# Optimization experiments

Hardware: AMD Instinct MI355X
Metric: run time of the kernel (lower is better)

Reference implementation:

```python
import jax, jax.numpy as jnp
import numpy as np

D_M = 1024
NUM_TOK = 4096


def setup_inputs() -> dict:
    key = jax.random.key(0)
    ks = jax.random.split(key, 7)
    mk = lambda k, shp: jax.random.normal(k, shp, dtype=jnp.float32) * 0.02
    return {
        "X": jax.random.normal(ks[0], (D_M, NUM_TOK), dtype=jnp.float32),
        "W_Q": mk(ks[1], (D_M, D_M)),
        "W_K": mk(ks[2], (D_M, D_M)),
        "W_V": mk(ks[3], (D_M, D_M)),
        "W_O": mk(ks[4], (D_M, D_M)),
        "mlp_in": mk(ks[5], (D_M, D_M)),
        "mlp_out": mk(ks[6], (D_M, D_M)),
    }


def reference(X, W_Q, W_K, W_V, W_O, mlp_in, mlp_out):
    # X: [d_m, num_tok]; module transposes to tokens-major [N, d]
    Xt = X.T  # [N, d]
    N = Xt.shape[0]
    Q = Xt @ W_Q  # [N, d]
    K = Xt @ W_K  # [N, d]
    scores = Q @ K.T  # [N, N] -- NOTE: no 1/sqrt(d) scaling, as in the original
    causal = jnp.tril(jnp.ones((N, N), dtype=bool))  # keep lower triangle incl. diag
    scores = jnp.where(causal, scores, -jnp.inf)
    A = jax.nn.softmax(scores, axis=-1)  # [N, N]
    # original applies W_V then W_O to X BEFORE the attention mix
    RH = (Xt @ W_V) @ W_O  # [N, d]
    Xt = Xt + A @ RH  # residual + attention
    h = jax.nn.relu(Xt @ mlp_in)  # [N, d] (hidden dim == d_m in original)
    Xt = Xt + h @ mlp_out  # residual + MLP
    return Xt.T  # back to [d_m, num_tok]
```

## Files before the change

### kernel.cpp

```cpp
#include <hip/hip_runtime.h>
#include <stdint.h>
#include <stddef.h>

using f16 = _Float16;
typedef __attribute__((ext_vector_type(8))) _Float16 f16x8;
typedef __attribute__((ext_vector_type(4))) float f32x4;

__device__ __forceinline__ void async_copy16(const f16* g, f16* l) {
    __builtin_amdgcn_global_load_lds(
        (const __attribute__((address_space(1))) void*)g,
        (__attribute__((address_space(3))) void*)l, 16, 0, 0);
}

template <int N>
__device__ __forceinline__ void wait_vmcnt() {
    if constexpr (N == 0)       asm volatile("s_waitcnt vmcnt(0)" ::: "memory");
    else if constexpr (N == 6)  asm volatile("s_waitcnt vmcnt(6)" ::: "memory");
    else if constexpr (N == 8)  asm volatile("s_waitcnt vmcnt(8)" ::: "memory");
}

__device__ __forceinline__ void hard_barrier() {
    __builtin_amdgcn_sched_barrier(0);
    __builtin_amdgcn_s_barrier();
    __builtin_amdgcn_sched_barrier(0);
}

__global__ __launch_bounds__(256)
void prep_w(const float* __restrict__ w0, const float* __restrict__ w1,
            const float* __restrict__ w2, const float* __restrict__ w3,
            const float* __restrict__ w4, const float* __restrict__ w5,
            f16* o0, f16* o1, f16* o2, f16* o3, f16* o4, f16* o5, int D) {
    __shared__ float tile[32][33];
    const int tx = threadIdx.x & 31, ty = threadIdx.x >> 5;
    const int b = blockIdx.x;
    const int z = b >> 10, r = b & 1023;
    const float* in = z == 0 ? w0 : z == 1 ? w1 : z == 2 ? w2 : z == 3 ? w3 : z == 4 ? w4 : w5;
    f16* out = z == 0 ? o0 : z == 1 ? o1 : z == 2 ? o2 : z == 3 ? o3 : z == 4 ? o4 : o5;
    const int c0 = (r & 31) * 32, r0 = (r >> 5) * 32;
    if (z < 3) {
#pragma unroll
        for (int j = 0; j < 4; j++) {
            size_t idx = (size_t)(r0 + ty + j * 8) * D + c0 + tx;
            out[idx] = (f16)in[idx];
        }
    } else {
#pragma unroll
        for (int j = 0; j < 4; j++)
            tile[ty + j * 8][tx] = in[(size_t)(r0 + ty + j * 8) * D + c0 + tx];
        __syncthreads();
#pragma unroll
        for (int j = 0; j < 4; j++)
            out[(size_t)(c0 + ty + j * 8) * D + r0 + tx] = (f16)tile[tx][ty + j * 8];
    }
}

__device__ __forceinline__ void body64db(
    f16* lds, const f16* __restrict__ A, const f16* __restrict__ B,
    f16* __restrict__ Ch, int m0, int n0, int N, int K, int lda) {
    const int t = threadIdx.x;
    const int lane = t & 63, wave = t >> 6;
    const int wm = (wave >> 1) * 32, wn = (wave & 1) * 32;
    const int lm = lane & 15, lq = lane >> 4;
    const int srow = t >> 2;
    const int gs = ((t & 3) ^ ((srow >> 1) & 3)) * 8;
    const int rs = (lq ^ ((lm >> 1) & 3)) * 8;

    auto stage = [&](f16* buf, int k0) {
#pragma unroll
        for (int r = 0; r < 4; r++)
            async_copy16(A + (size_t)(m0 + srow) * lda + k0 + r * 32 + gs,
                         buf + r * 2048 + t * 8);
#pragma unroll
        for (int r = 0; r < 4; r++)
            async_copy16(B + (size_t)(n0 + srow) * K + k0 + r * 32 + gs,
                         buf + 8192 + r * 2048 + t * 8);
    };

    f32x4 acc[2][2] = {};
    stage(lds, 0);
    __syncthreads();
    int cur = 0;
    for (int k0 = 0; k0 < K; k0 += 128) {
        f16* cb = lds + cur * 16384;
        if (k0 + 128 < K) stage(lds + (cur ^ 1) * 16384, k0 + 128);
#pragma unroll
        for (int kk = 0; kk < 4; kk++) {
            f16x8 af[2], bf[2];
#pragma unroll
            for (int i = 0; i < 2; i++)
                af[i] = *(const f16x8*)&cb[kk * 2048 + (wm + i * 16 + lm) * 32 + rs];
#pragma unroll
            for (int j = 0; j < 2; j++)
                bf[j] = *(const f16x8*)&cb[8192 + kk * 2048 + (wn + j * 16 + lm) * 32 + rs];
#pragma unroll
            for (int i = 0; i < 2; i++)
#pragma unroll
                for (int j = 0; j < 2; j++)
                    acc[i][j] = __builtin_amdgcn_mfma_f32_16x16x32_f16(
                        af[i], bf[j], acc[i][j], 0, 0, 0);
        }
        __syncthreads();
        cur ^= 1;
    }

#pragma unroll
    for (int i = 0; i < 2; i++) {
        const int row = m0 + wm + i * 16 + lq * 4;
#pragma unroll
        for (int j = 0; j < 2; j++) {
            const int col = n0 + wn + j * 16 + lm;
            f32x4 v = acc[i][j];
#pragma unroll
            for (int r = 0; r < 4; r++)
                Ch[(size_t)(row + r) * N + col] = (f16)v[r];
        }
    }
}

__global__ __launch_bounds__(256, 2)
void prepx_tiny(const float* __restrict__ X, f16* __restrict__ Xth,
                const f16* Wkh, const f16* Wqh, f16* GT,
                const f16* Wot, const f16* Wvh, f16* HT, int D, int NT) {
    __shared__ alignas(16) f16 smem[32768];
    int b = blockIdx.x;
    if (b < 4096) {
        float* tile = (float*)smem;
        const int tx = threadIdx.x & 31, ty = threadIdx.x >> 5;
        const int c0 = (b & 127) * 32, r0 = (b >> 7) * 32;
#pragma unroll
        for (int j = 0; j < 4; j++)
            tile[(ty + j * 8) * 33 + tx] = X[(size_t)(r0 + ty + j * 8) * NT + c0 + tx];
        __syncthreads();
#pragma unroll
        for (int j = 0; j < 4; j++)
            Xth[(size_t)(c0 + ty + j * 8) * D + r0 + tx] = (f16)tile[tx * 33 + ty + j * 8];
        return;
    }
    b -= 4096;
    if (b < 256)
        body64db(smem, Wkh, Wqh, GT, (b >> 4) * 64, (b & 15) * 64, 1024, 1024, 1024);
    else {
        const int r = b - 256;
        body64db(smem, Wot, Wvh, HT, (r >> 4) * 64, (r & 15) * 64, 1024, 1024, 1024);
    }
}

__global__ __launch_bounds__(256)
void softmax_rows(f16* __restrict__ A, int N) {
    const int row = blockIdx.x, len = row + 1;
    const int lim = ((row >> 7) + 1) << 7;
    f16* a = A + (size_t)row * N;
    __shared__ float red[256];
    const int t = threadIdx.x;

    float v[16];
    float mx = -1e30f;
#pragma unroll
    for (int j = 0; j < 2; j++) {
        const int c = (t + j * 256) * 8;
        if (c < len) {
            f16x8 x = *(const f16x8*)(a + c);
#pragma unroll
            for (int e = 0; e < 8; e++) {
                float f = (c + e < len) ? (float)x[e] : -1e30f;
                v[j * 8 + e] = f;
                mx = fmaxf(mx, f);
            }
        } else {
#pragma unroll
            for (int e = 0; e < 8; e++) v[j * 8 + e] = -1e30f;
        }
    }
    red[t] = mx; __syncthreads();
    for (int o = 128; o > 0; o >>= 1) { if (t < o) red[t] = fmaxf(red[t], red[t + o]); __syncthreads(); }
    mx = red[0]; __syncthreads();

    float sum = 0.f;
#pragma unroll
    for (int k = 0; k < 16; k++) {
        float e = (v[k] > -1e29f) ? __expf(v[k] - mx) : 0.0f;
        v[k] = e;
        sum += e;
    }
    red[t] = sum; __syncthreads();
    for (int o = 128; o > 0; o >>= 1) { if (t < o) red[t] += red[t + o]; __syncthreads(); }
    const float inv = 1.0f / red[0];
#pragma unroll
    for (int j = 0; j < 2; j++) {
        const int c = (t + j * 256) * 8;
        if (c < lim) {
            f16x8 o8;
#pragma unroll
            for (int e = 0; e < 8; e++) o8[e] = (f16)(v[j * 8 + e] * inv);
            *(f16x8*)(a + c) = o8;
        }
    }
}


__device__ __forceinline__ void body128sq(
    f16* lds, const f16* __restrict__ A, const f16* __restrict__ B,
    f16* __restrict__ Ch, int m0, int n0, int N, int K, int lda) {
    constexpr int BUF = 16384;
    const int t = threadIdx.x;
    const int lane = t & 63, wave = t >> 6;
    const int wm = (wave >> 1) * 64, wn = (wave & 1) * 64;
    const int lm = lane & 15, lq = lane >> 4;
    const int srow = t >> 2;
    const int gs = ((t & 3) ^ ((srow >> 1) & 3)) * 8;
    const int rs = (lq ^ ((lm >> 1) & 3)) * 8;

    f32x4 acc[4][4] = {};

    auto stage = [&](f16* buf, int k0) {
#pragma unroll
        for (int r = 0; r < 4; r++)
            async_copy16(A + (size_t)(m0 + (r & 1) * 64 + srow) * lda + k0 + (r >> 1) * 32 + gs,
                         buf + r * 2048 + t * 8);
#pragma unroll
        for (int r = 0; r < 4; r++)
            async_copy16(B + (size_t)(n0 + (r & 1) * 64 + srow) * K + k0 + (r >> 1) * 32 + gs,
                         buf + 8192 + r * 2048 + t * 8);
    };

    auto compute = [&](const f16* cb) {
#pragma unroll
        for (int kk = 0; kk < 2; kk++) {
            f16x8 af[4], bf[4];
#pragma unroll
            for (int i = 0; i < 4; i++)
                af[i] = *(const f16x8*)&cb[kk * 4096 + (wm + i * 16 + lm) * 32 + rs];
#pragma unroll
            for (int j = 0; j < 4; j++)
                bf[j] = *(const f16x8*)&cb[8192 + kk * 4096 + (wn + j * 16 + lm) * 32 + rs];
#pragma unroll
            for (int i = 0; i < 4; i++)
#pragma unroll
                for (int j = 0; j < 4; j++)
                    acc[i][j] = __builtin_amdgcn_mfma_f32_16x16x32_f16(
                        af[i], bf[j], acc[i][j], 0, 0, 0);
        }
    };

    const int NS = K >> 6;
    stage(lds, 0);
    for (int s = 0; s < NS; s++) {
        if (s + 1 < NS) {
            stage(lds + ((s + 1) & 1) * BUF, (s + 1) << 6);
            wait_vmcnt<8>();
        } else {
            wait_vmcnt<0>();
        }
        hard_barrier();
        compute(lds + (s & 1) * BUF);
        if (s + 1 < NS) hard_barrier();
    }

#pragma unroll
    for (int i = 0; i < 4; i++) {
        const int row = m0 + wm + i * 16 + lq * 4;
#pragma unroll
        for (int j = 0; j < 4; j++) {
            const int col = n0 + wn + j * 16 + lm;
            f32x4 v = acc[i][j];
#pragma unroll
            for (int r = 0; r < 4; r++)
                Ch[(size_t)(row + r) * N + col] = (f16)v[r];
        }
    }
}

template <int MODE>
__device__ __forceinline__ void body_nar2(
    f16* lds, const f16* __restrict__ A, const f16* __restrict__ B,
    float* __restrict__ Cf, f16* __restrict__ Ch, const f16* __restrict__ resid,
    int m0, int n0, int M, int N, int K, int lda, int Keff) {
    constexpr int ASZ = 128 * 64;
    constexpr int SSZ = ASZ + 64 * 64;
    const int t = threadIdx.x;
    const int lane = t & 63, wave = t >> 6;
    const int wm = (wave >> 1) * 64, wn = (wave & 1) * 32;
    const int lm = lane & 15, lq = lane >> 4;
    const int srow = t >> 2;
    const int gs = ((t & 3) ^ ((srow >> 1) & 3)) * 8;
    const int rs = (lq ^ ((lm >> 1) & 3)) * 8;

    f32x4 acc[4][2] = {};

    auto stage = [&](f16* buf, int k0) {
#pragma unroll
        for (int r = 0; r < 4; r++)
            async_copy16(A + (size_t)(m0 + (r & 1) * 64 + srow) * lda + k0 + (r >> 1) * 32 + gs,
                         buf + r * 2048 + t * 8);
#pragma unroll
        for (int r = 0; r < 2; r++)
            async_copy16(B + (size_t)(n0 + srow) * K + k0 + r * 32 + gs,
                         buf + ASZ + r * 2048 + t * 8);
    };

    auto compute = [&](const f16* cb) {
#pragma unroll
        for (int kk = 0; kk < 2; kk++) {
            f16x8 af[4], bf[2];
#pragma unroll
            for (int i = 0; i < 4; i++)
                af[i] = *(const f16x8*)&cb[kk * 4096 + (wm + i * 16 + lm) * 32 + rs];
#pragma unroll
            for (int j = 0; j < 2; j++)
                bf[j] = *(const f16x8*)&cb[ASZ + kk * 2048 + (wn + j * 16 + lm) * 32 + rs];
#pragma unroll
            for (int i = 0; i < 4; i++)
#pragma unroll
                for (int j = 0; j < 2; j++)
                    acc[i][j] = __builtin_amdgcn_mfma_f32_16x16x32_f16(
                        af[i], bf[j], acc[i][j], 0, 0, 0);
        }
    };

    stage(lds, 0);
    const int NS = Keff >> 6;
    for (int s = 0; s < NS; s++) {
        if (s + 1 < NS) {
            stage(lds + ((s + 1) & 1) * SSZ, (s + 1) << 6);
            wait_vmcnt<6>();
        } else {
            wait_vmcnt<0>();
        }
        hard_barrier();
        compute(lds + (s & 1) * SSZ);
        hard_barrier();
    }

#pragma unroll
    for (int i = 0; i < 4; i++) {
        const int row = m0 + wm + i * 16 + lq * 4;
#pragma unroll
        for (int j = 0; j < 2; j++) {
            const int col = n0 + wn + j * 16 + lm;
            f32x4 v = acc[i][j];
#pragma unroll
            for (int r = 0; r < 4; r++) {
                if (MODE == 0) {
                    Ch[(size_t)(row + r) * N + col] = (f16)v[r];
                } else if (MODE == 2) {
                    float o = v[r] + (float)resid[(size_t)(row + r) * N + col];
                    Ch[(size_t)(row + r) * N + col] = (f16)o;
                } else if (MODE == 3) {
                    Ch[(size_t)(row + r) * N + col] = (f16)fmaxf(v[r], 0.0f);
                } else {
                    float o = v[r] + (float)resid[(size_t)(row + r) * N + col];
                    Cf[(size_t)col * M + (row + r)] = o;
                }
            }
        }
    }
}

__global__ __launch_bounds__(256, 3)
void midq(const f16* Xth, const f16* GT, f16* Qp) {
    __shared__ alignas(16) f16 smem[24576];
    const int x = blockIdx.x & 7, s = blockIdx.x >> 3;
    const int m = x + 8 * (s >> 4), n = s & 15;
    body_nar2<0>(smem, Xth, GT, nullptr, Qp, nullptr,
                 m * 128, n * 64, 4096, 1024, 1024, 1024, 1024);
}

__global__ __launch_bounds__(256, 2)
void scores_midrh(const f16* Qp, const f16* Xth, f16* Af,
                  const f16* HT, f16* RHt) {
    __shared__ alignas(16) f16 smem[32768];
    int b = blockIdx.x;
    if (b < 528) {
        const int x = b & 7;
        int s = b >> 3;
        int m = 0, n = 0;
#pragma unroll
        for (int q = 3; q >= 0; q--) {
            const int mm = 8 * q + ((q & 1) ? 7 - x : x);
            if (s < mm + 1) { m = mm; n = s; break; }
            s -= mm + 1;
        }
        body128sq(smem, Qp, Xth, Af, m * 128, n * 128, 4096, 1024, 1024);
    } else {
        const int r = b - 528;
        const int x = r & 7;
        const int s = r >> 3;
        const int n = x + 8 * (s >> 3), m = s & 7;
        body128sq(smem, HT, Xth, RHt, m * 128, n * 128, 4096, 1024, 1024);
    }
}

template <int MODE, bool CAUSAL_K>
__global__ __launch_bounds__(256, 3)
void gemm_nar(const f16* __restrict__ A, const f16* __restrict__ B,
              float* __restrict__ Cf, f16* __restrict__ Ch,
              const f16* __restrict__ resid, int M, int N, int K, int lda) {
    __shared__ alignas(16) f16 smem[24576];
    const int x = blockIdx.x & 7, s = blockIdx.x >> 3;
    const int qs = s >> 4, n = s & 15;
    int m;
    if (CAUSAL_K) {
        const int q = (qs == 0) ? 3 : (qs == 1) ? 2 : (qs == 2) ? 0 : 1;
        m = 8 * q + ((q & 1) ? 7 - x : x);
    } else {
        m = x + 8 * qs;
    }
    const int m0 = m * 128, n0 = n * 64;
    int Keff = K;
    if (CAUSAL_K) {
        Keff = m0 + 128;
        if (Keff > K) Keff = K;
    }
    body_nar2<MODE>(smem, A, B, Cf, Ch, resid,
                    m0, n0, M, N, K, lda, Keff);
}

extern "C" void kernel_launch(void* const* d_in, const int* in_sizes, int n_in,
                              void* d_out, int out_size, void* d_ws, size_t ws_size,
                              hipStream_t stream) {
    const int D = 1024, NT = 4096;
    const float* X = (const float*)d_in[0];
    const float* W[6] = {(const float*)d_in[1], (const float*)d_in[2],
                         (const float*)d_in[3], (const float*)d_in[4],
                         (const float*)d_in[5], (const float*)d_in[6]};
    char* ws = (char*)d_ws;
    auto MB = [](size_t x) { return x << 20; };

    f16*   Xth  = (f16*)(ws + MB(0));
    f16*   Wqh  = (f16*)(ws + MB(8));
    f16*   Wkh  = (f16*)(ws + MB(10));
    f16*   Wvh  = (f16*)(ws + MB(12));
    f16*   Wot  = (f16*)(ws + MB(14));
    f16*   W4t  = (f16*)(ws + MB(16));
    f16*   W5t  = (f16*)(ws + MB(18));
    f16*   GT   = (f16*)(ws + MB(20));
    f16*   HT   = (f16*)(ws + MB(22));
    f16*   Qp   = (f16*)(ws + MB(24));
    f16*   Af   = (f16*)(ws + MB(32));
    f16*   RHt  = (f16*)(ws + MB(64));
    f16*   Y1h  = (f16*)(ws + MB(72));
    f16*   hb   = (f16*)(ws + MB(24));
    float* outF = (float*)d_out;

    prep_w<<<6144, 256, 0, stream>>>(W[0], W[1], W[2], W[3], W[4], W[5],
                                     Wqh, Wkh, Wvh, Wot, W4t, W5t, D);

    prepx_tiny<<<4608, 256, 0, stream>>>(X, Xth, Wkh, Wqh, GT, Wot, Wvh, HT,
                                         D, NT);

    midq<<<512, 256, 0, stream>>>(Xth, GT, Qp);

    scores_midrh<<<784, 256, 0, stream>>>(Qp, Xth, Af, HT, RHt);

    softmax_rows<<<NT, 256, 0, stream>>>(Af, NT);

    gemm_nar<2, true><<<512, 256, 0, stream>>>(
        Af, RHt, nullptr, Y1h, Xth, NT, D, NT, NT);

    gemm_nar<3, false><<<512, 256, 0, stream>>>(
        Y1h, W4t, nullptr, hb, nullptr, NT, D, D, D);

    gemm_nar<4, false><<<512, 256, 0, stream>>>(
        hb, W5t, outF, nullptr, Y1h, NT, D, D, D);
}
```

Baseline: 229.6 us.

## Use wave-per-row softmax, move MLP weight prep into scores kernel, adjust launch bounds

Softmax now assigns one 64-lane wavefront per row and reduces with shuffles instead of a 256-thread LDS tree with repeated block barriers. The exponentials are recomputed in the final pass so only raw half values need to stay in registers. The transpose/cast of the two MLP weights moves out of prep_w and into trailing blocks of the scores/RH kernel, where it can fill idle compute units. The occupancy hint for midq and gemm_nar drops from 3 to 2 blocks, which may let the compiler use more registers per thread at the cost of fewer resident blocks.

```diff
diff --git a/kernel.cpp b/kernel.cpp
--- a/kernel.cpp
+++ b/kernel.cpp
@@ -28,14 +28,13 @@
 __global__ __launch_bounds__(256)
 void prep_w(const float* __restrict__ w0, const float* __restrict__ w1,
             const float* __restrict__ w2, const float* __restrict__ w3,
-            const float* __restrict__ w4, const float* __restrict__ w5,
-            f16* o0, f16* o1, f16* o2, f16* o3, f16* o4, f16* o5, int D) {
+            f16* o0, f16* o1, f16* o2, f16* o3, int D) {
     __shared__ float tile[32][33];
     const int tx = threadIdx.x & 31, ty = threadIdx.x >> 5;
     const int b = blockIdx.x;
     const int z = b >> 10, r = b & 1023;
-    const float* in = z == 0 ? w0 : z == 1 ? w1 : z == 2 ? w2 : z == 3 ? w3 : z == 4 ? w4 : w5;
-    f16* out = z == 0 ? o0 : z == 1 ? o1 : z == 2 ? o2 : z == 3 ? o3 : z == 4 ? o4 : o5;
+    const float* in = z == 0 ? w0 : z == 1 ? w1 : z == 2 ? w2 : w3;
+    f16* out = z == 0 ? o0 : z == 1 ? o1 : z == 2 ? o2 : o3;
     const int c0 = (r & 31) * 32, r0 = (r >> 5) * 32;
     if (z < 3) {
 #pragma unroll
@@ -146,53 +145,60 @@
 }
 
 __global__ __launch_bounds__(256)
-void softmax_rows(f16* __restrict__ A, int N) {
-    const int row = blockIdx.x, len = row + 1;
+void softmax_waves(f16* __restrict__ A, int N) {
+    const int wid = threadIdx.x >> 6, lane = threadIdx.x & 63;
+    const int row = blockIdx.x * 4 + wid;
+    const int len = row + 1;
     const int lim = ((row >> 7) + 1) << 7;
     f16* a = A + (size_t)row * N;
-    __shared__ float red[256];
-    const int t = threadIdx.x;
-
-    float v[16];
+
+    f16x8 x[8];
+#pragma unroll
+    for (int c = 0; c < 8; c++)
+#pragma unroll
+        for (int e = 0; e < 8; e++) x[c][e] = (f16)0;
+
     float mx = -1e30f;
 #pragma unroll
-    for (int j = 0; j < 2; j++) {
-        const int c = (t + j * 256) * 8;
-        if (c < len) {
-            f16x8 x = *(const f16x8*)(a + c);
+    for (int c = 0; c < 8; c++) {
+        const int col = c * 512 + lane * 8;
+        if (col < len) {
+            x[c] = *(const f16x8*)(a + col);
+#pragma unroll
+            for (int e = 0; e < 8; e++)
+                if (col + e < len) mx = fmaxf(mx, (float)x[c][e]);
+        }
+    }
+#pragma unroll
+    for (int o = 32; o > 0; o >>= 1)
+        mx = fmaxf(mx, __shfl_xor(mx, o, 64));
+
+    float sum = 0.f;
+#pragma unroll
+    for (int c = 0; c < 8; c++) {
+        const int col = c * 512 + lane * 8;
+        if (col < len) {
+#pragma unroll
+            for (int e = 0; e < 8; e++)
+                if (col + e < len) sum += __expf((float)x[c][e] - mx);
+        }
+    }
+#pragma unroll
+    for (int o = 32; o > 0; o >>= 1)
+        sum += __shfl_xor(sum, o, 64);
+    const float inv = 1.0f / sum;
+
+#pragma unroll
+    for (int c = 0; c < 8; c++) {
+        const int col = c * 512 + lane * 8;
+        if (col < lim) {
+            f16x8 o8;
 #pragma unroll
             for (int e = 0; e < 8; e++) {
-                float f = (c + e < len) ? (float)x[e] : -1e30f;
-                v[j * 8 + e] = f;
-                mx = fmaxf(mx, f);
+                float v = (col + e < len) ? __expf((float)x[c][e] - mx) * inv : 0.0f;
+                o8[e] = (f16)v;
             }
-        } else {
-#pragma unroll
-            for (int e = 0; e < 8; e++) v[j * 8 + e] = -1e30f;
-        }
-    }
-    red[t] = mx; __syncthreads();
-    for (int o = 128; o > 0; o >>= 1) { if (t < o) red[t] = fmaxf(red[t], red[t + o]); __syncthreads(); }
-    mx = red[0]; __syncthreads();
-
-    float sum = 0.f;
-#pragma unroll
-    for (int k = 0; k < 16; k++) {
-        float e = (v[k] > -1e29f) ? __expf(v[k] - mx) : 0.0f;
-        v[k] = e;
-        sum += e;
-    }
-    red[t] = sum; __syncthreads();
-    for (int o = 128; o > 0; o >>= 1) { if (t < o) red[t] += red[t + o]; __syncthreads(); }
-    const float inv = 1.0f / red[0];
-#pragma unroll
-    for (int j = 0; j < 2; j++) {
-        const int c = (t + j * 256) * 8;
-        if (c < lim) {
-            f16x8 o8;
-#pragma unroll
-            for (int e = 0; e < 8; e++) o8[e] = (f16)(v[j * 8 + e] * inv);
-            *(f16x8*)(a + c) = o8;
+            *(f16x8*)(a + col) = o8;
         }
     }
 }
@@ -356,7 +362,7 @@
     }
 }
 
-__global__ __launch_bounds__(256, 3)
+__global__ __launch_bounds__(256, 2)
 void midq(const f16* Xth, const f16* GT, f16* Qp) {
     __shared__ alignas(16) f16 smem[24576];
     const int x = blockIdx.x & 7, s = blockIdx.x >> 3;
@@ -366,8 +372,10 @@
 }
 
 __global__ __launch_bounds__(256, 2)
-void scores_midrh(const f16* Qp, const f16* Xth, f16* Af,
-                  const f16* HT, f16* RHt) {
+void scores_midrh_w45(const f16* Qp, const f16* Xth, f16* Af,
+                      const f16* HT, f16* RHt,
+                      const float* __restrict__ w4, const float* __restrict__ w5,
+                      f16* W4t, f16* W5t, int D) {
     __shared__ alignas(16) f16 smem[32768];
     int b = blockIdx.x;
     if (b < 528) {
@@ -381,17 +389,34 @@
             s -= mm + 1;
         }
         body128sq(smem, Qp, Xth, Af, m * 128, n * 128, 4096, 1024, 1024);
-    } else {
+        return;
+    }
+    if (b < 784) {
         const int r = b - 528;
         const int x = r & 7;
         const int s = r >> 3;
         const int n = x + 8 * (s >> 3), m = s & 7;
         body128sq(smem, HT, Xth, RHt, m * 128, n * 128, 4096, 1024, 1024);
-    }
+        return;
+    }
+    float* tile = (float*)smem;
+    const int tx = threadIdx.x & 31, ty = threadIdx.x >> 5;
+    const int r = b - 784;
+    const float* in = (r < 1024) ? w4 : w5;
+    f16* out = (r < 1024) ? W4t : W5t;
+    const int rr = r & 1023;
+    const int c0 = (rr & 31) * 32, r0 = (rr >> 5) * 32;
+#pragma unroll
+    for (int j = 0; j < 4; j++)
+        tile[(ty + j * 8) * 33 + tx] = in[(size_t)(r0 + ty + j * 8) * D + c0 + tx];
+    __syncthreads();
+#pragma unroll
+    for (int j = 0; j < 4; j++)
+        out[(size_t)(c0 + ty + j * 8) * D + r0 + tx] = (f16)tile[tx * 33 + ty + j * 8];
 }
 
 template <int MODE, bool CAUSAL_K>
-__global__ __launch_bounds__(256, 3)
+__global__ __launch_bounds__(256, 2)
 void gemm_nar(const f16* __restrict__ A, const f16* __restrict__ B,
               float* __restrict__ Cf, f16* __restrict__ Ch,
               const f16* __restrict__ resid, int M, int N, int K, int lda) {
@@ -442,17 +467,18 @@
     f16*   hb   = (f16*)(ws + MB(24));
     float* outF = (float*)d_out;
 
-    prep_w<<<6144, 256, 0, stream>>>(W[0], W[1], W[2], W[3], W[4], W[5],
-                                     Wqh, Wkh, Wvh, Wot, W4t, W5t, D);
+    prep_w<<<4096, 256, 0, stream>>>(W[0], W[1], W[2], W[3],
+                                     Wqh, Wkh, Wvh, Wot, D);
 
     prepx_tiny<<<4608, 256, 0, stream>>>(X, Xth, Wkh, Wqh, GT, Wot, Wvh, HT,
                                          D, NT);
 
     midq<<<512, 256, 0, stream>>>(Xth, GT, Qp);
 
-    scores_midrh<<<784, 256, 0, stream>>>(Qp, Xth, Af, HT, RHt);
-
-    softmax_rows<<<NT, 256, 0, stream>>>(Af, NT);
+    scores_midrh_w45<<<2832, 256, 0, stream>>>(Qp, Xth, Af, HT, RHt,
+                                               W[4], W[5], W4t, W5t, D);
+
+    softmax_waves<<<1024, 256, 0, stream>>>(Af, NT);
 
     gemm_nar<2, true><<<512, 256, 0, stream>>>(
         Af, RHt, nullptr, Y1h, Xth, NT, D, NT, NT);
```

Result: no change. 230.9 us (+0.5%).
